# Kernel tuning notes

Measured on AMD Instinct MI355X. Metric: run time of the kernel, lower is better.

The kernel has to match this reference:

```python
import jax, jax.numpy as jnp
import numpy as np

# Constants from mode='only_tv': gamma_l1=gamma_dwt=beta=lambda_l1=lambda_dwt=sigma=0,
# so u_l1,u_dwt,z,eta_l1,eta_dwt,rho stay identically zero and drop out of the math.
GAMMA_TV = 2.0
ALPHA = 5.0
LAMBDA_TV = 1e-4
N_ITER = 200


def soft_thresh(v, t):
    return jnp.sign(v) * jnp.maximum(jnp.abs(v) - t, 0.0)


def setup_inputs() -> dict:
    key = jax.random.key(0)
    k1, k2, k3 = jax.random.split(key, 3)
    target = jax.random.normal(k1, (4096, 64), dtype=jnp.float32)  # B spectra of K bands
    A = jax.random.normal(k2, (9, 64), dtype=jnp.float32) * 0.1     # (M=9 channels, K=64 bands)
    x0 = jax.random.normal(k3, (4096, 64), dtype=jnp.float32)       # replaces randn_like(target)
    return {"target": target, "A": A, "x0": x0}


def reference(target, A, x0):
    # target, x0: (B, K) batch of per-sample length-K vectors; A: (M, K)
    K = A.shape[1]
    AT = A.T  # (K, M)
    I = jnp.eye(K, dtype=A.dtype)
    Delta = jnp.roll(I, 1, axis=1) - I          # (K, K)
    DtD = Delta.T @ Delta
    inv_item = jnp.linalg.inv(AT @ A + GAMMA_TV * DtD + ALPHA * I)  # (K, K)

    # b = A @ x  per sample  ->  (B, M);  AT @ b per sample -> (B, K)
    b = target @ A.T
    ATb = b @ A

    # per-sample Delta @ v, batched over rows -> v_mat @ Delta.T
    def D(v):
        return v @ Delta.T

    eta_tv0 = jnp.zeros_like(x0)
    tau0 = jnp.zeros_like(x0)

    def step(carry, _):
        x, eta_tv, tau = carry
        u_tv = soft_thresh(D(x) + eta_tv / GAMMA_TV, LAMBDA_TV / GAMMA_TV)
        w = jnp.maximum(x + tau / ALPHA, 0.0)
        # note: torch's matmul(z_tv, DeltaT) on a vector equals Delta @ z_tv -> batched D(.)
        resid = ATb + D(GAMMA_TV * u_tv - eta_tv) + ALPHA * w - tau
        x = resid @ inv_item.T  # per-sample inv_item @ resid
        eta_tv = eta_tv + GAMMA_TV * (D(x) - u_tv)
        tau = tau + ALPHA * (x - w)
        return (x, eta_tv, tau), None

    (x, _, _), _ = jax.lax.scan(step, (x0, eta_tv0, tau0), None, length=N_ITER)
    return x
```

## Files before the change

### kernel.cpp

```cpp
#include <hip/hip_runtime.h>

#define NSAMP 4096
#define NITER 200

__global__ __launch_bounds__(256) void setup_woodbury(const float* __restrict__ A,
                                                      float* __restrict__ mperm) {
  __shared__ double lamr[64];
  __shared__ float binv[64];
  __shared__ float P[9][64];
  __shared__ float Q[9][64];
  __shared__ double W[9][18];
  __shared__ float Mfull[64][64];
  const int tid = threadIdx.x;
  const double TWO_PI = 6.283185307179586476925286766559;

  double cb = 0.0;
  if (tid < 64) {
    cb = cos(TWO_PI * (double)tid / 64.0);
    lamr[tid] = 1.0 / (9.0 - 4.0 * cb);
  }
  __syncthreads();
  if (tid < 64) {
    double cm1 = 1.0, c0 = cb;
    double acc = lamr[0] + cb * lamr[1];
#pragma unroll 16
    for (int m = 2; m < 64; ++m) {
      double c = 2.0 * cb * c0 - cm1;
      cm1 = c0;
      c0 = c;
      acc += c * lamr[m];
    }
    binv[tid] = (float)(acc / 64.0);
  }
  __syncthreads();

  for (int e = tid; e < 9 * 64; e += 256) {
    int m = e >> 6, i = e & 63;
    double acc = 0.0;
#pragma unroll 16
    for (int k = 0; k < 64; ++k)
      acc += (double)A[m * 64 + k] * (double)binv[(k - i) & 63];
    P[m][i] = (float)acc;
  }
  __syncthreads();

  if (tid < 81) {
    int m = tid / 9, n = tid % 9;
    double acc = (m == n) ? 1.0 : 0.0;
#pragma unroll 16
    for (int i = 0; i < 64; ++i)
      acc += (double)P[m][i] * (double)A[n * 64 + i];
    W[m][n] = acc;
    W[m][n + 9] = (m == n) ? 1.0 : 0.0;
  }
  __syncthreads();

  {
    const int r9 = tid / 18, c9 = tid % 18;
    const bool act = (tid < 162);
    for (int k = 0; k < 9; ++k) {
      double pv = 1.0, f = 0.0, wkc = 0.0;
      if (act) {
        pv = W[k][k];
        f = W[r9][k];
        wkc = W[k][c9];
      }
      __syncthreads();
      if (act) {
        double nk = wkc / pv;
        W[r9][c9] = (r9 == k) ? nk : fma(-f, nk, W[r9][c9]);
      }
      __syncthreads();
    }
  }

  for (int e = tid; e < 9 * 64; e += 256) {
    int m = e >> 6, j = e & 63;
    double acc = 0.0;
#pragma unroll
    for (int n = 0; n < 9; ++n) acc += W[m][n + 9] * (double)P[n][j];
    Q[m][j] = (float)acc;
  }
  __syncthreads();

  for (int e = tid; e < 64 * 64; e += 256) {
    int i = e >> 6, j = e & 63;
    float acc = binv[(i - j) & 63];
#pragma unroll
    for (int m = 0; m < 9; ++m) acc = fmaf(-P[m][i], Q[m][j], acc);
    Mfull[i][j] = acc;
  }
  __syncthreads();

  const int lidw = tid & 63;
  int dpp1;
  asm volatile(
      "s_nop 4\n\t"
      "v_mov_b32_dpp %0, %1 row_ror:1 row_mask:0xf bank_mask:0xf\n\t"
      "s_nop 4"
      : "=v"(dpp1)
      : "v"(lidw));
  const int lane0val = __builtin_amdgcn_readfirstlane(dpp1);
  const int dir = (lane0val == 1) ? 1 : -1;

  for (int e = tid; e < 64 * 64; e += 256) {
    int li = e >> 6, k = e & 63;
    int j;
    if (k < 48) {
      int st = k >> 4, t = k & 15;
      int xs = (st == 0) ? 0 : (st == 1 ? 16 : 48);
      int q = (li & 48) | (((li & 15) + dir * t + 16) & 15);
      j = q ^ xs;
    } else {
      int t = (k - 48) >> 2, ee = k & 3;
      j = ((li & 48) ^ 32) + 4 * ((((li >> 4) & 3) + t) & 3) + ee;
    }
    mperm[li * 64 + k] = Mfull[li][j];
  }
}

#define DPL(op, acc, rr, mm, rot) \
  op " " acc ", " rr ", " mm " row_ror:" #rot " row_mask:0xf bank_mask:0xf\n\t"

__global__ __launch_bounds__(256)
void admm_kernel(const float* __restrict__ target, const float* __restrict__ A,
                 const float* __restrict__ x0, const float* __restrict__ mperm,
                 float* __restrict__ out) {
  __shared__ __align__(16) float rbuf[4][64];
  const int tid = threadIdx.x;
  const int wid = tid >> 6;
  const int lane = tid & 63;
  const int s = blockIdx.x * 4 + wid;

  float t = target[s * 64 + lane];
  float atbv = 0.f;
#pragma unroll
  for (int m = 0; m < 9; ++m) {
    float a = A[m * 64 + lane];
    float p = t * a;
#pragma unroll
    for (int off = 32; off; off >>= 1) p += __shfl_xor(p, off, 64);
    atbv = fmaf(a, p, atbv);
  }

  const float* mrow = mperm + (size_t)lane * 64;
  unsigned int rb_base = (unsigned int)(uintptr_t)(&rbuf[wid][0]);
  unsigned int a_w = rb_base + lane * 4;
  unsigned int a_nxt = ((lane + 1) & 63) * 4;
  unsigned int a_x32 = (lane ^ 32) * 4;
  unsigned int g = (lane >> 4) & 3;
  unsigned int base3 = rb_base + (((lane & 48) ^ 32) << 2);
  unsigned int aq0 = base3 + (((g + 0) & 3) << 4);
  unsigned int aq1 = base3 + (((g + 1) & 3) << 4);
  unsigned int aq2 = base3 + (((g + 2) & 3) << 4);
  unsigned int aq3 = base3 + (((g + 3) & 3) << 4);
  float xin = x0[s * 64 + lane];
  float xout;
  int cnt_s;
  const int smask = 0x7fffffff;
  const float sthr = 5e-5f, sc02 = 0.2f, sc5 = 5.0f;

  asm volatile(
      "s_mov_b32 m0, -1\n\t"
      "global_load_dwordx4 v[64:67],   %[mp], off\n\t"
      "global_load_dwordx4 v[68:71],   %[mp], off offset:16\n\t"
      "global_load_dwordx4 v[72:75],   %[mp], off offset:32\n\t"
      "global_load_dwordx4 v[76:79],   %[mp], off offset:48\n\t"
      "global_load_dwordx4 v[80:83],   %[mp], off offset:64\n\t"
      "global_load_dwordx4 v[84:87],   %[mp], off offset:80\n\t"
      "global_load_dwordx4 v[88:91],   %[mp], off offset:96\n\t"
      "global_load_dwordx4 v[92:95],   %[mp], off offset:112\n\t"
      "global_load_dwordx4 v[96:99],   %[mp], off offset:128\n\t"
      "global_load_dwordx4 v[100:103], %[mp], off offset:144\n\t"
      "global_load_dwordx4 v[104:107], %[mp], off offset:160\n\t"
      "global_load_dwordx4 v[108:111], %[mp], off offset:176\n\t"
      "global_load_dwordx4 v[112:115], %[mp], off offset:192\n\t"
      "global_load_dwordx4 v[116:119], %[mp], off offset:208\n\t"
      "global_load_dwordx4 v[120:123], %[mp], off offset:224\n\t"
      "global_load_dwordx4 v[124:127], %[mp], off offset:240\n\t"
      "v_mov_b32 v32, %[xin]\n\t"
      "v_mov_b32 v36, %[atb]\n\t"
      "v_mov_b32 v33, 0\n\t"
      "v_mov_b32 v34, 0\n\t"
      "ds_bpermute_b32 v45, %[anx], v32\n\t"
      "s_waitcnt lgkmcnt(0)\n\t"
      "v_sub_f32 v35, v45, v32\n\t"
      "s_movk_i32 %[cnt], 200\n\t"
      "s_waitcnt vmcnt(0)\n\t"
      "1:\n\t"
      "v_fma_f32 v40, 0.5, v33, v35\n\t"
      "v_and_b32 v41, %[msk], v40\n\t"
      "v_subrev_f32 v41, %[thr], v41\n\t"
      "v_max_f32 v41, 0, v41\n\t"
      "v_bfi_b32 v42, %[msk], v41, v40\n\t"
      "v_fma_f32 v43, %[c02], v34, v32\n\t"
      "v_max_f32 v43, 0, v43\n\t"
      "v_fma_f32 v40, 2.0, v42, -v33\n\t"
      "ds_bpermute_b32 v45, %[anx], v40\n\t"
      "v_fma_f32 v44, %[c5], v43, v36\n\t"
      "v_sub_f32 v44, v44, v34\n\t"
      "v_sub_f32 v44, v44, v40\n\t"
      "s_waitcnt lgkmcnt(0)\n\t"
      "v_add_f32 v44, v44, v45\n\t"
      "ds_swizzle_b32 v45, v44 offset:0x401F\n\t"
      "ds_write_b32 %[aw], v44\n\t"
      "ds_read_b128 v[48:51], %[aq0]\n\t"
      "ds_read_b128 v[52:55], %[aq1]\n\t"
      "ds_read_b128 v[56:59], %[aq2]\n\t"
      "ds_read_b128 v[60:63], %[aq3]\n\t"
      "v_mul_f32 v37, v44, v64\n\t"
      DPL("v_mul_f32",  "v38", "v44", "v65", 1)
      DPL("v_mul_f32",  "v39", "v44", "v66", 2)
      DPL("v_mul_f32",  "v40", "v44", "v67", 3)
      DPL("v_fmac_f32", "v37", "v44", "v68", 4)
      DPL("v_fmac_f32", "v38", "v44", "v69", 5)
      DPL("v_fmac_f32", "v39", "v44", "v70", 6)
      DPL("v_fmac_f32", "v40", "v44", "v71", 7)
      DPL("v_fmac_f32", "v37", "v44", "v72", 8)
      DPL("v_fmac_f32", "v38", "v44", "v73", 9)
      DPL("v_fmac_f32", "v39", "v44", "v74", 10)
      DPL("v_fmac_f32", "v40", "v44", "v75", 11)
      DPL("v_fmac_f32", "v37", "v44", "v76", 12)
      DPL("v_fmac_f32", "v38", "v44", "v77", 13)
      DPL("v_fmac_f32", "v39", "v44", "v78", 14)
      DPL("v_fmac_f32", "v40", "v44", "v79", 15)
      "s_waitcnt lgkmcnt(5)\n\t"
      "ds_bpermute_b32 v46, %[a32], v45\n\t"
      "s_nop 1\n\t"
      "v_fmac_f32 v37, v45, v80\n\t"
      DPL("v_fmac_f32", "v38", "v45", "v81", 1)
      DPL("v_fmac_f32", "v39", "v45", "v82", 2)
      DPL("v_fmac_f32", "v40", "v45", "v83", 3)
      DPL("v_fmac_f32", "v37", "v45", "v84", 4)
      DPL("v_fmac_f32", "v38", "v45", "v85", 5)
      DPL("v_fmac_f32", "v39", "v45", "v86", 6)
      DPL("v_fmac_f32", "v40", "v45", "v87", 7)
      DPL("v_fmac_f32", "v37", "v45", "v88", 8)
      DPL("v_fmac_f32", "v38", "v45", "v89", 9)
      DPL("v_fmac_f32", "v39", "v45", "v90", 10)
      DPL("v_fmac_f32", "v40", "v45", "v91", 11)
      DPL("v_fmac_f32", "v37", "v45", "v92", 12)
      DPL("v_fmac_f32", "v38", "v45", "v93", 13)
      DPL("v_fmac_f32", "v39", "v45", "v94", 14)
      DPL("v_fmac_f32", "v40", "v45", "v95", 15)
      "s_waitcnt lgkmcnt(0)\n\t"
      "s_nop 1\n\t"
      "v_fmac_f32 v37, v46, v96\n\t"
      DPL("v_fmac_f32", "v38", "v46", "v97", 1)
      DPL("v_fmac_f32", "v39", "v46", "v98", 2)
      DPL("v_fmac_f32", "v40", "v46", "v99", 3)
      DPL("v_fmac_f32", "v37", "v46", "v100", 4)
      DPL("v_fmac_f32", "v38", "v46", "v101", 5)
      DPL("v_fmac_f32", "v39", "v46", "v102", 6)
      DPL("v_fmac_f32", "v40", "v46", "v103", 7)
      DPL("v_fmac_f32", "v37", "v46", "v104", 8)
      DPL("v_fmac_f32", "v38", "v46", "v105", 9)
      DPL("v_fmac_f32", "v39", "v46", "v106", 10)
      DPL("v_fmac_f32", "v40", "v46", "v107", 11)
      DPL("v_fmac_f32", "v37", "v46", "v108", 12)
      DPL("v_fmac_f32", "v38", "v46", "v109", 13)
      DPL("v_fmac_f32", "v39", "v46", "v110", 14)
      DPL("v_fmac_f32", "v40", "v46", "v111", 15)
      "v_pk_mul_f32 v[44:45], v[112:113], v[48:49]\n\t"
      "v_pk_mul_f32 v[46:47], v[114:115], v[50:51]\n\t"
      "v_pk_fma_f32 v[44:45], v[116:117], v[52:53], v[44:45]\n\t"
      "v_pk_fma_f32 v[46:47], v[118:119], v[54:55], v[46:47]\n\t"
      "v_pk_fma_f32 v[44:45], v[120:121], v[56:57], v[44:45]\n\t"
      "v_pk_fma_f32 v[46:47], v[122:123], v[58:59], v[46:47]\n\t"
      "v_pk_fma_f32 v[44:45], v[124:125], v[60:61], v[44:45]\n\t"
      "v_pk_fma_f32 v[46:47], v[126:127], v[62:63], v[46:47]\n\t"
      "v_add_f32 v37, v37, v38\n\t"
      "v_add_f32 v39, v39, v40\n\t"
      "v_pk_add_f32 v[44:45], v[44:45], v[46:47]\n\t"
      "v_add_f32 v37, v37, v39\n\t"
      "v_add_f32 v44, v44, v45\n\t"
      "v_add_f32 v32, v37, v44\n\t"
      "ds_bpermute_b32 v45, %[anx], v32\n\t"
      "v_sub_f32 v41, v32, v43\n\t"
      "v_fma_f32 v34, %[c5], v41, v34\n\t"
      "s_waitcnt lgkmcnt(0)\n\t"
      "v_sub_f32 v35, v45, v32\n\t"
      "v_sub_f32 v41, v35, v42\n\t"
      "v_fma_f32 v33, 2.0, v41, v33\n\t"
      "s_sub_u32 %[cnt], %[cnt], 1\n\t"
      "s_cmp_lg_u32 %[cnt], 0\n\t"
      "s_cbranch_scc1 1b\n\t"
      "v_mov_b32 %[xout], v32\n\t"
      : [xout] "=v"(xout), [cnt] "=&s"(cnt_s)
      : [mp] "v"(mrow), [aw] "v"(a_w), [anx] "v"(a_nxt), [a32] "v"(a_x32),
        [aq0] "v"(aq0), [aq1] "v"(aq1), [aq2] "v"(aq2), [aq3] "v"(aq3),
        [xin] "v"(xin), [atb] "v"(atbv),
        [msk] "s"(smask), [thr] "s"(sthr), [c02] "s"(sc02), [c5] "s"(sc5)
      : "memory", "scc",
        "v32","v33","v34","v35","v36","v37","v38","v39","v40","v41","v42","v43",
        "v44","v45","v46","v47","v48","v49","v50","v51","v52","v53","v54","v55",
        "v56","v57","v58","v59","v60","v61","v62","v63","v64","v65","v66","v67",
        "v68","v69","v70","v71","v72","v73","v74","v75","v76","v77","v78","v79",
        "v80","v81","v82","v83","v84","v85","v86","v87","v88","v89","v90","v91",
        "v92","v93","v94","v95","v96","v97","v98","v99","v100","v101","v102",
        "v103","v104","v105","v106","v107","v108","v109","v110","v111","v112",
        "v113","v114","v115","v116","v117","v118","v119","v120","v121","v122",
        "v123","v124","v125","v126","v127");

  out[s * 64 + lane] = xout;
}

extern "C" void kernel_launch(void* const* d_in, const int* in_sizes, int n_in,
                              void* d_out, int out_size, void* d_ws, size_t ws_size,
                              hipStream_t stream) {
  const float* target = (const float*)d_in[0];
  const float* A = (const float*)d_in[1];
  const float* x0 = (const float*)d_in[2];
  float* out = (float*)d_out;
  float* mperm = (float*)d_ws;

  setup_woodbury<<<1, 256, 0, stream>>>(A, mperm);
  admm_kernel<<<NSAMP / 4, 256, 0, stream>>>(target, A, x0, mperm, out);
}
```

Measured before the change: 195.9 us.

## Fuse Woodbury setup into ADMM kernel and keep the permuted matrix in LDS

Merges the single-block setup kernel into the main ADMM kernel, so every block recomputes the 64x64 permuted inverse matrix in shared memory. Each lane then loads its matrix row with LDS reads instead of global loads. This removes the second launch and the serialized one-block setup stage before the main solve. The cost is that the setup work is repeated in every block and each block needs about 40KB of LDS. The padded row stride of 65 floats also gives row addresses that are not 16-byte aligned for the b128 LDS reads.

```diff
diff --git a/kernel.cpp b/kernel.cpp
--- a/kernel.cpp
+++ b/kernel.cpp
@@ -3,15 +3,26 @@
 #define NSAMP 4096
 #define NITER 200
 
-__global__ __launch_bounds__(256) void setup_woodbury(const float* __restrict__ A,
-                                                      float* __restrict__ mperm) {
-  __shared__ double lamr[64];
-  __shared__ float binv[64];
-  __shared__ float P[9][64];
-  __shared__ float Q[9][64];
-  __shared__ double W[9][18];
-  __shared__ float Mfull[64][64];
+#define DPL(op, acc, rr, mm, rot) \
+  op " " acc ", " rr ", " mm " row_ror:" #rot " row_mask:0xf bank_mask:0xf\n\t"
+
+__global__ __launch_bounds__(256)
+void admm_fused(const float* __restrict__ target, const float* __restrict__ A,
+                const float* __restrict__ x0, float* __restrict__ out) {
+  __shared__ __align__(16) char smem[40208];
+  float (*Mfull)[64] = (float(*)[64])(smem);
+  float* Mperm       = (float*)(smem + 16384);
+  float (*rbuf)[64]  = (float(*)[64])(smem + 33024);
+  double* lamr       = (double*)(smem + 33024);
+  float* binv        = (float*)(smem + 34048);
+  float (*P)[64]     = (float(*)[64])(smem + 34304);
+  float (*Q)[64]     = (float(*)[64])(smem + 36608);
+  double (*W)[18]    = (double(*)[18])(smem + 38912);
+
   const int tid = threadIdx.x;
+  const int wid = tid >> 6;
+  const int lane = tid & 63;
+  const int s = blockIdx.x * 4 + wid;
   const double TWO_PI = 6.283185307179586476925286766559;
 
   double cb = 0.0;
@@ -92,16 +103,14 @@
   }
   __syncthreads();
 
-  const int lidw = tid & 63;
   int dpp1;
   asm volatile(
       "s_nop 4\n\t"
       "v_mov_b32_dpp %0, %1 row_ror:1 row_mask:0xf bank_mask:0xf\n\t"
       "s_nop 4"
       : "=v"(dpp1)
-      : "v"(lidw));
-  const int lane0val = __builtin_amdgcn_readfirstlane(dpp1);
-  const int dir = (lane0val == 1) ? 1 : -1;
+      : "v"(lane));
+  const int dir = (__builtin_amdgcn_readfirstlane(dpp1) == 1) ? 1 : -1;
 
   for (int e = tid; e < 64 * 64; e += 256) {
     int li = e >> 6, k = e & 63;
@@ -115,22 +124,9 @@
       int t = (k - 48) >> 2, ee = k & 3;
       j = ((li & 48) ^ 32) + 4 * ((((li >> 4) & 3) + t) & 3) + ee;
     }
-    mperm[li * 64 + k] = Mfull[li][j];
-  }
-}
-
-#define DPL(op, acc, rr, mm, rot) \
-  op " " acc ", " rr ", " mm " row_ror:" #rot " row_mask:0xf bank_mask:0xf\n\t"
-
-__global__ __launch_bounds__(256)
-void admm_kernel(const float* __restrict__ target, const float* __restrict__ A,
-                 const float* __restrict__ x0, const float* __restrict__ mperm,
-                 float* __restrict__ out) {
-  __shared__ __align__(16) float rbuf[4][64];
-  const int tid = threadIdx.x;
-  const int wid = tid >> 6;
-  const int lane = tid & 63;
-  const int s = blockIdx.x * 4 + wid;
+    Mperm[li * 65 + k] = Mfull[li][j];
+  }
+  __syncthreads();
 
   float t = target[s * 64 + lane];
   float atbv = 0.f;
@@ -143,13 +139,13 @@
     atbv = fmaf(a, p, atbv);
   }
 
-  const float* mrow = mperm + (size_t)lane * 64;
-  unsigned int rb_base = (unsigned int)(uintptr_t)(&rbuf[wid][0]);
-  unsigned int a_w = rb_base + lane * 4;
+  unsigned int mprm = (unsigned int)(uintptr_t)(Mperm + lane * 65);
+  unsigned int rb = (unsigned int)(uintptr_t)(&rbuf[wid][0]);
+  unsigned int a_w = rb + lane * 4;
   unsigned int a_nxt = ((lane + 1) & 63) * 4;
   unsigned int a_x32 = (lane ^ 32) * 4;
   unsigned int g = (lane >> 4) & 3;
-  unsigned int base3 = rb_base + (((lane & 48) ^ 32) << 2);
+  unsigned int base3 = rb + (((lane & 48) ^ 32) << 2);
   unsigned int aq0 = base3 + (((g + 0) & 3) << 4);
   unsigned int aq1 = base3 + (((g + 1) & 3) << 4);
   unsigned int aq2 = base3 + (((g + 2) & 3) << 4);
@@ -162,22 +158,22 @@
 
   asm volatile(
       "s_mov_b32 m0, -1\n\t"
-      "global_load_dwordx4 v[64:67],   %[mp], off\n\t"
-      "global_load_dwordx4 v[68:71],   %[mp], off offset:16\n\t"
-      "global_load_dwordx4 v[72:75],   %[mp], off offset:32\n\t"
-      "global_load_dwordx4 v[76:79],   %[mp], off offset:48\n\t"
-      "global_load_dwordx4 v[80:83],   %[mp], off offset:64\n\t"
-      "global_load_dwordx4 v[84:87],   %[mp], off offset:80\n\t"
-      "global_load_dwordx4 v[88:91],   %[mp], off offset:96\n\t"
-      "global_load_dwordx4 v[92:95],   %[mp], off offset:112\n\t"
-      "global_load_dwordx4 v[96:99],   %[mp], off offset:128\n\t"
-      "global_load_dwordx4 v[100:103], %[mp], off offset:144\n\t"
-      "global_load_dwordx4 v[104:107], %[mp], off offset:160\n\t"
-      "global_load_dwordx4 v[108:111], %[mp], off offset:176\n\t"
-      "global_load_dwordx4 v[112:115], %[mp], off offset:192\n\t"
-      "global_load_dwordx4 v[116:119], %[mp], off offset:208\n\t"
-      "global_load_dwordx4 v[120:123], %[mp], off offset:224\n\t"
-      "global_load_dwordx4 v[124:127], %[mp], off offset:240\n\t"
+      "ds_read_b128 v[64:67],   %[mprm]\n\t"
+      "ds_read_b128 v[68:71],   %[mprm] offset:16\n\t"
+      "ds_read_b128 v[72:75],   %[mprm] offset:32\n\t"
+      "ds_read_b128 v[76:79],   %[mprm] offset:48\n\t"
+      "ds_read_b128 v[80:83],   %[mprm] offset:64\n\t"
+      "ds_read_b128 v[84:87],   %[mprm] offset:80\n\t"
+      "ds_read_b128 v[88:91],   %[mprm] offset:96\n\t"
+      "ds_read_b128 v[92:95],   %[mprm] offset:112\n\t"
+      "ds_read_b128 v[96:99],   %[mprm] offset:128\n\t"
+      "ds_read_b128 v[100:103], %[mprm] offset:144\n\t"
+      "ds_read_b128 v[104:107], %[mprm] offset:160\n\t"
+      "ds_read_b128 v[108:111], %[mprm] offset:176\n\t"
+      "ds_read_b128 v[112:115], %[mprm] offset:192\n\t"
+      "ds_read_b128 v[116:119], %[mprm] offset:208\n\t"
+      "ds_read_b128 v[120:123], %[mprm] offset:224\n\t"
+      "ds_read_b128 v[124:127], %[mprm] offset:240\n\t"
       "v_mov_b32 v32, %[xin]\n\t"
       "v_mov_b32 v36, %[atb]\n\t"
       "v_mov_b32 v33, 0\n\t"
@@ -186,7 +182,6 @@
       "s_waitcnt lgkmcnt(0)\n\t"
       "v_sub_f32 v35, v45, v32\n\t"
       "s_movk_i32 %[cnt], 200\n\t"
-      "s_waitcnt vmcnt(0)\n\t"
       "1:\n\t"
       "v_fma_f32 v40, 0.5, v33, v35\n\t"
       "v_and_b32 v41, %[msk], v40\n\t"
@@ -287,7 +282,7 @@
       "s_cbranch_scc1 1b\n\t"
       "v_mov_b32 %[xout], v32\n\t"
       : [xout] "=v"(xout), [cnt] "=&s"(cnt_s)
-      : [mp] "v"(mrow), [aw] "v"(a_w), [anx] "v"(a_nxt), [a32] "v"(a_x32),
+      : [mprm] "v"(mprm), [aw] "v"(a_w), [anx] "v"(a_nxt), [a32] "v"(a_x32),
         [aq0] "v"(aq0), [aq1] "v"(aq1), [aq2] "v"(aq2), [aq3] "v"(aq3),
         [xin] "v"(xin), [atb] "v"(atbv),
         [msk] "s"(smask), [thr] "s"(sthr), [c02] "s"(sc02), [c5] "s"(sc5)
@@ -312,8 +307,6 @@
   const float* A = (const float*)d_in[1];
   const float* x0 = (const float*)d_in[2];
   float* out = (float*)d_out;
-  float* mperm = (float*)d_ws;
-
-  setup_woodbury<<<1, 256, 0, stream>>>(A, mperm);
-  admm_kernel<<<NSAMP / 4, 256, 0, stream>>>(target, A, x0, mperm, out);
+
+  admm_fused<<<NSAMP / 4, 256, 0, stream>>>(target, A, x0, out);
 }
```

New measurement: 194.9 us. About the same (-0.5%).
